# Performance work log

Hardware: AMD Instinct MI355X
Metric: run time of the kernel (lower is better)

Reference implementation:

```python
import jax, jax.numpy as jnp
import numpy as np
from jax import lax

D_MODEL = 512
NUM_HEADS = 8
HEADDIM = D_MODEL // NUM_HEADS      # 64
EXPAND = 2
D_INNER = EXPAND * D_MODEL          # 1024
D_STATE = 64
NGROUPS = 1
KCONV = 4                           # window_size -> depthwise conv kernel
NHEADS = D_INNER // HEADDIM         # 16 SSM heads
D_FF = 2048
CONV_DIM = D_INNER + 2 * NGROUPS * D_STATE          # 1152 (x, B, C)
D_IN_PROJ = 2 * D_INNER + 2 * NGROUPS * D_STATE + NHEADS  # 2192 (z, x, B, C, dt)
EPS = 1e-6


def _rmsnorm(x, eps=EPS):
    return x * lax.rsqrt(jnp.mean(x * x, axis=-1, keepdims=True) + eps)


def _silu(x):
    return x * jax.nn.sigmoid(x)


def _ssm_scan(xs, dt, A, Bm, Cm):
    # xs: [B,L,H,P], dt: [B,L,H], A: [H], Bm/Cm: [B,L,N]  (ngroups=1 broadcast over heads)
    dA = jnp.exp(dt * A)                 # [B,L,H] decay per step
    dBx = dt[..., None] * xs             # [B,L,H,P] input contribution
    h0 = jnp.zeros((xs.shape[0], xs.shape[2], xs.shape[3], Bm.shape[2]), xs.dtype)

    def step(h, t):
        dA_t, dBx_t, B_t, C_t = t        # [B,H],[B,H,P],[B,N],[B,N]
        h = dA_t[..., None, None] * h + dBx_t[..., None] * B_t[:, None, None, :]
        y = jnp.einsum('bhpn,bn->bhp', h, C_t)
        return h, y

    _, ys = lax.scan(step, h0, (dA.transpose(1, 0, 2), dBx.transpose(1, 0, 2, 3),
                                Bm.transpose(1, 0, 2), Cm.transpose(1, 0, 2)))
    return ys.transpose(1, 0, 2, 3)      # [B,L,H,P]


def setup_inputs() -> dict:
    key = jax.random.key(0)
    ks = jax.random.split(key, 12)
    B, L = 8, 2048
    s = 0.02
    inp = {
        'x': jax.random.normal(ks[0], (B, L, D_MODEL), jnp.float32),
        'mask': jnp.ones((B, L), jnp.float32),
        'W_in': jax.random.normal(ks[1], (D_MODEL, D_IN_PROJ), jnp.float32) * s,
        'conv_w': jax.random.normal(ks[2], (CONV_DIM, KCONV), jnp.float32) * 0.1,
        'conv_b': jnp.zeros((CONV_DIM,), jnp.float32),
        'dt_bias': jax.random.normal(ks[3], (NHEADS,), jnp.float32) * 0.1,
        'A_log': jnp.log(jnp.arange(1, NHEADS + 1, dtype=jnp.float32)),
        'D': jnp.ones((NHEADS,), jnp.float32),
        'norm_w': jnp.ones((D_INNER,), jnp.float32),
        'W_out': jax.random.normal(ks[4], (D_INNER, D_MODEL), jnp.float32) * s,
        'W1': jax.random.normal(ks[5], (D_MODEL, D_FF), jnp.float32) * s,
        'b1': jnp.zeros((D_FF,), jnp.float32),
        'W2': jax.random.normal(ks[6], (D_FF, D_MODEL), jnp.float32) * s,
        'b2': jnp.zeros((D_MODEL,), jnp.float32),
    }
    return inp


def reference(x, mask, W_in, conv_w, conv_b, dt_bias, A_log, D, norm_w, W_out, W1, b1, W2, b2):
    B, L, _ = x.shape
    x = x * mask[..., None]
    u = _rmsnorm(x)

    zxbcdt = u @ W_in                                   # [B,L,2192]
    z = zxbcdt[..., :D_INNER]
    xBC = zxbcdt[..., D_INNER:D_INNER + CONV_DIM]
    dt = zxbcdt[..., D_INNER + CONV_DIM:]               # [B,L,H]

    # causal depthwise conv1d, kernel KCONV
    pad = jnp.pad(xBC, ((0, 0), (KCONV - 1, 0), (0, 0)))
    xBC = sum(pad[:, i:i + L, :] * conv_w[:, i] for i in range(KCONV)) + conv_b
    xBC = _silu(xBC) * mask[..., None]

    xs = xBC[..., :D_INNER].reshape(B, L, NHEADS, HEADDIM)
    Bm = xBC[..., D_INNER:D_INNER + D_STATE]            # [B,L,N] (ngroups=1)
    Cm = xBC[..., D_INNER + D_STATE:]

    dt = jax.nn.softplus(dt + dt_bias)
    A = -jnp.exp(A_log)                                 # [H]

    # bidirectional (non-causal) selective scan: forward + reversed scans
    y_f = _ssm_scan(xs, dt, A, Bm, Cm)
    y_b = _ssm_scan(xs[:, ::-1], dt[:, ::-1], A, Bm[:, ::-1], Cm[:, ::-1])[:, ::-1]
    y = y_f + y_b + D[None, None, :, None] * xs         # [B,L,H,P]
    y = y.reshape(B, L, D_INNER)

    # gated RMSNorm then output projection
    y = _rmsnorm(y * _silu(z)) * norm_w
    m = y @ W_out                                       # mamba2 output, [B,L,D]

    x = m + m                                           # x = x + dropout1(x) with x := mamba out
    h = _rmsnorm(x)
    x = x + (jax.nn.gelu(h @ W1 + b1) @ W2 + b2)        # x + mlp(norm2(x))
    return (x, m, dt, z)
```

## Files before the change

kernel.cpp:

```cpp
#include <hip/hip_runtime.h>
#include <cstdint>
#include <cstddef>

#define L_SEQ   2048
#define NROWS   16384
#define D_MODEL 512
#define D_INNER 1024
#define D_STATE 64
#define NHEADS  16
#define CONV_DIM 1152
#define D_IN_PROJ 2192
#define D_FF 2048
#define EPS 1e-6f

typedef __bf16 bf16_t;
typedef __bf16 bf16x8 __attribute__((ext_vector_type(8)));
typedef float  f32x4  __attribute__((ext_vector_type(4)));

#define OFF_WT_IN    0ull
#define OFF_WT_OUT   2244608ull
#define OFF_W1T      3293184ull
#define OFF_W2T      5390336ull
#define OFF_U        7487488ull
#define OFF_XBC_RAW  24264704ull
#define OFF_XBC_CONV 99762176ull
#define OFF_Y2       175259648ull
#define OFF_YN       242368512ull

__device__ __forceinline__ void gl_lds16(const void* g, void* s) {
  __builtin_amdgcn_global_load_lds(
      (__attribute__((address_space(1))) void*)(void*)g,
      (__attribute__((address_space(3))) void*)s, 16, 0, 0);
}

__device__ __forceinline__ float block_sum256(float v, float* red) {
#pragma unroll
  for (int o = 32; o > 0; o >>= 1) v += __shfl_xor(v, o, 64);
  int w = threadIdx.x >> 6;
  if ((threadIdx.x & 63) == 0) red[w] = v;
  __syncthreads();
  return red[0] + red[1] + red[2] + red[3];
}

__device__ __forceinline__ float softplus_f(float x) {
  return (x > 20.f) ? x : log1pf(expf(x));
}
__device__ __forceinline__ float silu_f(float x) {
  return x / (1.f + expf(-x));
}
__device__ __forceinline__ float gelu_tanh_f(float x) {
  float x3 = x * x * x;
  return 0.5f * x * (1.f + tanhf(0.7978845608f * (x + 0.044715f * x3)));
}

__global__ __launch_bounds__(256) void prep_weights_kernel(
    const float* __restrict__ W_in, const float* __restrict__ W_out,
    const float* __restrict__ W1, const float* __restrict__ W2,
    bf16_t* __restrict__ wt_in, bf16_t* __restrict__ wt_out,
    bf16_t* __restrict__ w1t, bf16_t* __restrict__ w2t) {
  const int S1 = D_IN_PROJ * 512;
  const int S2 = 512 * 1024;
  const int S3 = 2048 * 512;
  const int S4 = 512 * 2048;
  const int total = S1 + S2 + S3 + S4;
  for (int i = blockIdx.x * 256 + threadIdx.x; i < total; i += gridDim.x * 256) {
    if (i < S1) {
      int n = i / 512, k = i - n * 512;
      wt_in[i] = (bf16_t)W_in[k * D_IN_PROJ + n];
    } else if (i < S1 + S2) {
      int j = i - S1; int n = j >> 10, k = j & 1023;
      wt_out[j] = (bf16_t)W_out[k * 512 + n];
    } else if (i < S1 + S2 + S3) {
      int j = i - S1 - S2; int n = j >> 9, k = j & 511;
      w1t[j] = (bf16_t)W1[k * 2048 + n];
    } else {
      int j = i - S1 - S2 - S3; int n = j >> 11, k = j & 2047;
      w2t[j] = (bf16_t)W2[k * 512 + n];
    }
  }
}

__global__ __launch_bounds__(256) void rmsnorm_in_kernel(
    const float* __restrict__ x, const float* __restrict__ mask,
    bf16_t* __restrict__ u) {
  __shared__ float red[4];
  int row = blockIdx.x;
  float mk = mask[row];
  const float* xr = x + (size_t)row * 512;
  float v0 = xr[threadIdx.x] * mk;
  float v1 = xr[threadIdx.x + 256] * mk;
  float ss = block_sum256(v0 * v0 + v1 * v1, red);
  float r = rsqrtf(ss * (1.f / 512.f) + EPS);
  bf16_t* ur = u + (size_t)row * 512;
  ur[threadIdx.x] = (bf16_t)(v0 * r);
  ur[threadIdx.x + 256] = (bf16_t)(v1 * r);
}

__global__ __launch_bounds__(256) void rmsnorm2_kernel(
    const float* __restrict__ m, bf16_t* __restrict__ h) {
  __shared__ float red[4];
  int row = blockIdx.x;
  const float* mr = m + (size_t)row * 512;
  float v0 = 2.f * mr[threadIdx.x];
  float v1 = 2.f * mr[threadIdx.x + 256];
  float ss = block_sum256(v0 * v0 + v1 * v1, red);
  float r = rsqrtf(ss * (1.f / 512.f) + EPS);
  bf16_t* hr = h + (size_t)row * 512;
  hr[threadIdx.x] = (bf16_t)(v0 * r);
  hr[threadIdx.x + 256] = (bf16_t)(v1 * r);
}

template <int EPI>
__global__ __launch_bounds__(256, 2) void gemm_kernel(
    const bf16_t* __restrict__ A, const bf16_t* __restrict__ Bt,
    int M, int N, int K,
    float* __restrict__ o0, float* __restrict__ o1, float* __restrict__ o2,
    bf16_t* __restrict__ ob, const float* __restrict__ bias,
    const float* __restrict__ extra) {
  __shared__ bf16_t As[128 * 32];
  __shared__ bf16_t Bs[128 * 32];
  const int tid = threadIdx.x;
  const int lane = tid & 63;
  const int w = tid >> 6;
  const int tileM = blockIdx.y * 128;
  const int tileN = blockIdx.x * 128;

  f32x4 acc[4][4] = {};

  const int wm = (w >> 1) * 64;
  const int wn = (w & 1) * 64;
  const int fr = lane & 15;
  const int fk = (lane >> 4) * 8;

  for (int k0 = 0; k0 < K; k0 += 32) {
    __syncthreads();
#pragma unroll
    for (int i = 0; i < 2; ++i) {
      int rloc = w * 32 + i * 16 + (lane >> 2);
      int cb = (lane & 3) * 16;
      const char* ga = (const char*)(A + (size_t)(tileM + rloc) * K + k0) + cb;
      gl_lds16(ga, (void*)&As[(w * 32 + i * 16) * 32]);
      int rn = tileN + rloc;
      if (rn >= N) rn = N - 1;
      const char* gb = (const char*)(Bt + (size_t)rn * K + k0) + cb;
      gl_lds16(gb, (void*)&Bs[(w * 32 + i * 16) * 32]);
    }
    __syncthreads();

    bf16x8 av[4], bv[4];
#pragma unroll
    for (int i = 0; i < 4; ++i)
      av[i] = *(const bf16x8*)&As[(wm + i * 16 + fr) * 32 + fk];
#pragma unroll
    for (int j = 0; j < 4; ++j)
      bv[j] = *(const bf16x8*)&Bs[(wn + j * 16 + fr) * 32 + fk];
#pragma unroll
    for (int i = 0; i < 4; ++i)
#pragma unroll
      for (int j = 0; j < 4; ++j)
        acc[i][j] = __builtin_amdgcn_mfma_f32_16x16x32_bf16(av[i], bv[j], acc[i][j], 0, 0, 0);
  }

  const int cn = lane & 15;
  const int r0 = (lane >> 4) * 4;
#pragma unroll
  for (int i = 0; i < 4; ++i) {
#pragma unroll
    for (int j = 0; j < 4; ++j) {
      int gn = tileN + wn + j * 16 + cn;
      if (gn >= N) continue;
#pragma unroll
      for (int r = 0; r < 4; ++r) {
        int gm = tileM + wm + i * 16 + r0 + r;
        float v = acc[i][j][r];
        if (EPI == 0) {
          o0[(size_t)gm * N + gn] = v;
        } else if (EPI == 1) {
          if (gn < D_INNER) {
            o0[(size_t)gm * D_INNER + gn] = v;
          } else if (gn < D_INNER + CONV_DIM) {
            o1[(size_t)gm * CONV_DIM + (gn - D_INNER)] = v;
          } else {
            int hh = gn - (D_INNER + CONV_DIM);
            o2[(size_t)gm * NHEADS + hh] = softplus_f(v + bias[hh]);
          }
        } else if (EPI == 2) {
          ob[(size_t)gm * N + gn] = (bf16_t)gelu_tanh_f(v + bias[gn]);
        } else if (EPI == 3) {
          o0[(size_t)gm * N + gn] = v + bias[gn] + 2.f * extra[(size_t)gm * N + gn];
        }
      }
    }
  }
}

__global__ __launch_bounds__(384) void conv_silu_kernel(
    const float* __restrict__ xbc_raw, const float* __restrict__ conv_w,
    const float* __restrict__ conv_b, const float* __restrict__ mask,
    float* __restrict__ xbc_conv) {
  int row = blockIdx.x;
  int t = row & (L_SEQ - 1);
  float mk = mask[row];
#pragma unroll
  for (int k = 0; k < 3; ++k) {
    int c = threadIdx.x + k * 384;
    float4 wv = ((const float4*)conv_w)[c];
    float acc = conv_b[c];
    if (t >= 3) acc += wv.x * xbc_raw[(size_t)(row - 3) * CONV_DIM + c];
    if (t >= 2) acc += wv.y * xbc_raw[(size_t)(row - 2) * CONV_DIM + c];
    if (t >= 1) acc += wv.z * xbc_raw[(size_t)(row - 1) * CONV_DIM + c];
    acc += wv.w * xbc_raw[(size_t)row * CONV_DIM + c];
    xbc_conv[(size_t)row * CONV_DIM + c] = silu_f(acc) * mk;
  }
}


__global__ __launch_bounds__(256) void scan_chunk_kernel(
    const float* __restrict__ xbc, const float* __restrict__ dt_all,
    const float* __restrict__ A_log,
    bf16_t* __restrict__ y2, bf16_t* __restrict__ Tc_buf,
    float* __restrict__ la_buf) {
  const int bid = blockIdx.x;
  const int c = bid & 31, h = (bid >> 5) & 15, b = (bid >> 9) & 7, dir = bid >> 12;
  const float A_h = -expf(A_log[h]);
  const int tid = threadIdx.x, w = tid >> 6, lane = tid & 63;
  const int fr = lane & 15, fk = (lane >> 4) * 8;

  __shared__ __align__(16) bf16_t sB[64][72];
  __shared__ __align__(16) bf16_t sC[64][72];
  __shared__ __align__(16) bf16_t sXt[64][72];
  __shared__ __align__(16) bf16_t sBwt[64][72];
  __shared__ float sLa[64], sDt[64], sW[64];

  const size_t base = (size_t)b * L_SEQ;
#define ROWOF(i) (base + (size_t)(dir ? (L_SEQ - 1 - (c * 64 + (i))) : (c * 64 + (i))))

  if (tid < 64) sDt[tid] = dt_all[ROWOF(tid) * NHEADS + h];

  float bB[16];
#pragma unroll
  for (int r = 0; r < 16; ++r) {
    int i = w * 16 + r;
    const float* src = xbc + ROWOF(i) * CONV_DIM;
    float xv = src[h * 64 + lane];
    float bv = src[D_INNER + lane];
    float cv = src[D_INNER + D_STATE + lane];
    bB[r] = bv;
    sB[i][lane] = (bf16_t)bv;
    sC[i][lane] = (bf16_t)cv;
    sXt[lane][i] = (bf16_t)xv;
  }
  __syncthreads();

  if (w == 0) {
    float v = sDt[lane] * A_h;
#pragma unroll
    for (int d = 1; d < 64; d <<= 1) {
      float o = __shfl_up(v, d, 64);
      if (lane >= d) v += o;
    }
    sLa[lane] = v;
    float la63 = __shfl(v, 63, 64);
    sW[lane] = __expf(la63 - v) * sDt[lane];
  }
  __syncthreads();

#pragma unroll
  for (int r = 0; r < 16; ++r) {
    int i = w * 16 + r;
    sBwt[lane][i] = (bf16_t)(bB[r] * sW[i]);
  }
  if (tid < 64) la_buf[(size_t)bid * 64 + tid] = sLa[tid];

  f32x4 acc1[4] = {};
#pragma unroll
  for (int k0 = 0; k0 < 64; k0 += 32) {
    bf16x8 bv = *(const bf16x8*)&sC[w * 16 + fr][k0 + fk];
#pragma unroll
    for (int mi = 0; mi < 4; ++mi) {
      if (mi <= w) {
        bf16x8 av = *(const bf16x8*)&sB[mi * 16 + fr][k0 + fk];
        acc1[mi] = __builtin_amdgcn_mfma_f32_16x16x32_bf16(av, bv, acc1[mi], 0, 0, 0);
      }
    }
  }
  __syncthreads();

  {
    bf16_t (*sM)[72] = sB;
    float la_t = sLa[w * 16 + fr];
    int t = w * 16 + fr;
#pragma unroll
    for (int mi = 0; mi < 4; ++mi) {
#pragma unroll
      for (int r = 0; r < 4; ++r) {
        int s = mi * 16 + (lane >> 4) * 4 + r;
        float mv = 0.f;
        if (s <= t) mv = acc1[mi][r] * __expf(la_t - sLa[s]) * sDt[s];
        sM[t][s] = (bf16_t)mv;
      }
    }
  }

  f32x4 acc3[4] = {};
#pragma unroll
  for (int k0 = 0; k0 < 64; k0 += 32) {
    bf16x8 bv = *(const bf16x8*)&sBwt[w * 16 + fr][k0 + fk];
#pragma unroll
    for (int mi = 0; mi < 4; ++mi) {
      bf16x8 av = *(const bf16x8*)&sXt[mi * 16 + fr][k0 + fk];
      acc3[mi] = __builtin_amdgcn_mfma_f32_16x16x32_bf16(av, bv, acc3[mi], 0, 0, 0);
    }
  }
  __syncthreads();

  f32x4 acc2[4] = {};
  {
    bf16_t (*sM)[72] = sB;
#pragma unroll
    for (int k0 = 0; k0 < 64; k0 += 32) {
      bf16x8 bv = *(const bf16x8*)&sXt[w * 16 + fr][k0 + fk];
#pragma unroll
      for (int mi = 0; mi < 4; ++mi) {
        bf16x8 av = *(const bf16x8*)&sM[mi * 16 + fr][k0 + fk];
        acc2[mi] = __builtin_amdgcn_mfma_f32_16x16x32_bf16(av, bv, acc2[mi], 0, 0, 0);
      }
    }
  }

  bf16_t* yout = y2 + (size_t)dir * NROWS * D_INNER;
  bf16_t* tco = Tc_buf + (size_t)bid * 4096;
#pragma unroll
  for (int mi = 0; mi < 4; ++mi) {
#pragma unroll
    for (int r = 0; r < 4; ++r) {
      int rowl = mi * 16 + (lane >> 4) * 4 + r;
      int coll = w * 16 + fr;
      yout[ROWOF(rowl) * D_INNER + h * 64 + coll] = (bf16_t)acc2[mi][r];
      tco[rowl * 64 + coll] = (bf16_t)acc3[mi][r];
    }
  }
#undef ROWOF
}

__global__ __launch_bounds__(256) void state_prefix_kernel(
    const float* __restrict__ la_buf, bf16_t* __restrict__ Tc_buf) {
  const int g = blockIdx.x >> 1;
  const int e0 = (blockIdx.x & 1) * 2048 + threadIdx.x * 8;
  bf16_t* tc = Tc_buf + (size_t)g * 32 * 4096 + e0;
  const float* la63 = la_buf + (size_t)g * 32 * 64 + 63;
  float S[8] = {};
  for (int cc = 0; cc < 32; ++cc) {
    bf16x8 t = *(const bf16x8*)(tc + (size_t)cc * 4096);
    float d = __expf(la63[cc * 64]);
    bf16_t sb[8];
#pragma unroll
    for (int j = 0; j < 8; ++j) sb[j] = (bf16_t)S[j];
    *(bf16x8*)(tc + (size_t)cc * 4096) = *(bf16x8*)sb;
    const bf16_t* tp = (const bf16_t*)&t;
#pragma unroll
    for (int j = 0; j < 8; ++j) S[j] = d * S[j] + (float)tp[j];
  }
}

__global__ __launch_bounds__(256) void ystate_kernel(
    const float* __restrict__ xbc, const bf16_t* __restrict__ S_buf,
    const float* __restrict__ la_buf, bf16_t* __restrict__ y2) {
  const int bid = blockIdx.x;
  const int c = bid & 31, h = (bid >> 5) & 15, b = (bid >> 9) & 7, dir = bid >> 12;
  const int tid = threadIdx.x, w = tid >> 6, lane = tid & 63;
  const int fr = lane & 15, fk = (lane >> 4) * 8;
  const size_t base = (size_t)b * L_SEQ;

  const bf16_t* Sp = S_buf + (size_t)bid * 4096;
  f32x4 acc[4] = {};
#pragma unroll
  for (int k0 = 0; k0 < 64; k0 += 32) {
    bf16x8 bv = *(const bf16x8*)&Sp[(w * 16 + fr) * 64 + k0 + fk];
#pragma unroll
    for (int mi = 0; mi < 4; ++mi) {
      int t = c * 64 + mi * 16 + fr;
      int tr = dir ? (L_SEQ - 1 - t) : t;
      const float* cp = xbc + (base + tr) * CONV_DIM + D_INNER + D_STATE + k0 + fk;
      bf16_t av[8];
#pragma unroll
      for (int j = 0; j < 8; ++j) av[j] = (bf16_t)cp[j];
      acc[mi] = __builtin_amdgcn_mfma_f32_16x16x32_bf16(*(bf16x8*)av, bv, acc[mi], 0, 0, 0);
    }
  }
  const float* la = la_buf + (size_t)bid * 64;
  bf16_t* yout = y2 + (size_t)dir * NROWS * D_INNER;
  const int p = w * 16 + fr;
#pragma unroll
  for (int mi = 0; mi < 4; ++mi) {
#pragma unroll
    for (int r = 0; r < 4; ++r) {
      int tl = mi * 16 + (lane >> 4) * 4 + r;
      int t = c * 64 + tl;
      int tr = dir ? (L_SEQ - 1 - t) : t;
      size_t g = (base + tr) * D_INNER + h * 64 + p;
      float v = acc[mi][r] * __expf(la[tl]);
      yout[g] = (bf16_t)((float)yout[g] + v);
    }
  }
}

__global__ __launch_bounds__(256) void combine_kernel(
    const bf16_t* __restrict__ y2, const float* __restrict__ xbc_conv,
    const float* __restrict__ z, const float* __restrict__ Dp,
    const float* __restrict__ norm_w, bf16_t* __restrict__ yn) {
  __shared__ float red[4];
  int row = blockIdx.x;
  const bf16_t* yf = y2 + (size_t)row * D_INNER;
  const bf16_t* yb = y2 + (size_t)NROWS * D_INNER + (size_t)row * D_INNER;
  const float* xs = xbc_conv + (size_t)row * CONV_DIM;
  const float* zr = z + (size_t)row * D_INNER;

  float g[4];
  float ss = 0.f;
#pragma unroll
  for (int k = 0; k < 4; ++k) {
    int c = threadIdx.x + k * 256;
    float v = (float)yf[c] + (float)yb[c] + Dp[c >> 6] * xs[c];
    float gg = v * silu_f(zr[c]);
    g[k] = gg;
    ss += gg * gg;
  }
  ss = block_sum256(ss, red);
  float r = rsqrtf(ss * (1.f / 1024.f) + EPS);
  bf16_t* yr = yn + (size_t)row * D_INNER;
#pragma unroll
  for (int k = 0; k < 4; ++k) {
    int c = threadIdx.x + k * 256;
    yr[c] = (bf16_t)(g[k] * r * norm_w[c]);
  }
}

extern "C" void kernel_launch(void* const* d_in, const int* in_sizes, int n_in,
                              void* d_out, int out_size, void* d_ws, size_t ws_size,
                              hipStream_t stream) {
  const float* x       = (const float*)d_in[0];
  const float* mask    = (const float*)d_in[1];
  const float* W_in    = (const float*)d_in[2];
  const float* conv_w  = (const float*)d_in[3];
  const float* conv_b  = (const float*)d_in[4];
  const float* dt_bias = (const float*)d_in[5];
  const float* A_log   = (const float*)d_in[6];
  const float* Dp      = (const float*)d_in[7];
  const float* norm_w  = (const float*)d_in[8];
  const float* W_out   = (const float*)d_in[9];
  const float* W1      = (const float*)d_in[10];
  const float* b1      = (const float*)d_in[11];
  const float* W2      = (const float*)d_in[12];
  const float* b2      = (const float*)d_in[13];

  float* out_x  = (float*)d_out;
  float* out_m  = out_x + (size_t)NROWS * 512;
  float* out_dt = out_m + (size_t)NROWS * 512;
  float* out_z  = out_dt + (size_t)NROWS * NHEADS;

  char* ws = (char*)d_ws;
  bf16_t* wt_in    = (bf16_t*)(ws + OFF_WT_IN);
  bf16_t* wt_out   = (bf16_t*)(ws + OFF_WT_OUT);
  bf16_t* w1t      = (bf16_t*)(ws + OFF_W1T);
  bf16_t* w2t      = (bf16_t*)(ws + OFF_W2T);
  bf16_t* u_bf     = (bf16_t*)(ws + OFF_U);
  float*  xbc_raw  = (float*)(ws + OFF_XBC_RAW);
  float*  xbc_conv = (float*)(ws + OFF_XBC_CONV);
  bf16_t* y2       = (bf16_t*)(ws + OFF_Y2);
  bf16_t* yn       = (bf16_t*)(ws + OFF_YN);
  bf16_t* h_bf     = u_bf;
  bf16_t* gelu_bf  = (bf16_t*)(ws + OFF_XBC_RAW);
  bf16_t* Tc_buf   = (bf16_t*)(ws + OFF_XBC_RAW);
  float*  la_buf   = (float*)(ws + OFF_U);

  prep_weights_kernel<<<14624, 256, 0, stream>>>(W_in, W_out, W1, W2, wt_in, wt_out, w1t, w2t);
  rmsnorm_in_kernel<<<NROWS, 256, 0, stream>>>(x, mask, u_bf);
  gemm_kernel<1><<<dim3(18, 128), 256, 0, stream>>>(u_bf, wt_in, NROWS, D_IN_PROJ, 512,
                                                    out_z, xbc_raw, out_dt, nullptr, dt_bias, nullptr);
  conv_silu_kernel<<<NROWS, 384, 0, stream>>>(xbc_raw, conv_w, conv_b, mask, xbc_conv);
  scan_chunk_kernel<<<8192, 256, 0, stream>>>(xbc_conv, out_dt, A_log, y2, Tc_buf, la_buf);
  state_prefix_kernel<<<512, 256, 0, stream>>>(la_buf, Tc_buf);
  ystate_kernel<<<8192, 256, 0, stream>>>(xbc_conv, Tc_buf, la_buf, y2);
  combine_kernel<<<NROWS, 256, 0, stream>>>(y2, xbc_conv, out_z, Dp, norm_w, yn);
  gemm_kernel<0><<<dim3(4, 128), 256, 0, stream>>>(yn, wt_out, NROWS, 512, 1024,
                                                   out_m, nullptr, nullptr, nullptr, nullptr, nullptr);
  rmsnorm2_kernel<<<NROWS, 256, 0, stream>>>(out_m, h_bf);
  gemm_kernel<2><<<dim3(16, 128), 256, 0, stream>>>(h_bf, w1t, NROWS, D_FF, 512,
                                                    nullptr, nullptr, nullptr, gelu_bf, b1, nullptr);
  gemm_kernel<3><<<dim3(4, 128), 256, 0, stream>>>(gelu_bf, w2t, NROWS, 512, D_FF,
                                                   out_x, nullptr, nullptr, nullptr, b2, out_m);
}
```

Baseline: 728.9 us.

## Stage C tile in LDS, reuse across four heads, and vectorize y updates

The ystate kernel now loads the C tile for each chunk into shared memory once, converts it to bf16, and reuses it for four heads per block. Previously each block reread and converted C from global memory for a single head. Results are staged through an LDS buffer so the read-modify-write of y2 uses coalesced 16-byte accesses instead of scattered scalar bf16 accesses. The grid shrinks by a factor of four, which lowers parallelism and adds extra barriers per head.

```diff
diff --git a/kernel.cpp b/kernel.cpp
--- a/kernel.cpp
+++ b/kernel.cpp
@@ -15,6 +15,7 @@
 
 typedef __bf16 bf16_t;
 typedef __bf16 bf16x8 __attribute__((ext_vector_type(8)));
+typedef __bf16 bf16x4 __attribute__((ext_vector_type(4)));
 typedef float  f32x4  __attribute__((ext_vector_type(4)));
 
 #define OFF_WT_IN    0ull
@@ -367,40 +368,72 @@
     const float* __restrict__ xbc, const bf16_t* __restrict__ S_buf,
     const float* __restrict__ la_buf, bf16_t* __restrict__ y2) {
   const int bid = blockIdx.x;
-  const int c = bid & 31, h = (bid >> 5) & 15, b = (bid >> 9) & 7, dir = bid >> 12;
+  const int hg = bid & 3, c = (bid >> 2) & 31, b = (bid >> 7) & 7, dir = bid >> 10;
   const int tid = threadIdx.x, w = tid >> 6, lane = tid & 63;
   const int fr = lane & 15, fk = (lane >> 4) * 8;
   const size_t base = (size_t)b * L_SEQ;
 
-  const bf16_t* Sp = S_buf + (size_t)bid * 4096;
-  f32x4 acc[4] = {};
-#pragma unroll
-  for (int k0 = 0; k0 < 64; k0 += 32) {
-    bf16x8 bv = *(const bf16x8*)&Sp[(w * 16 + fr) * 64 + k0 + fk];
+  __shared__ __align__(16) bf16_t sC[64][72];
+  __shared__ __align__(16) float  sYf[64][72];
+  __shared__ float sEla[64];
+
+#pragma unroll
+  for (int uu = 0; uu < 4; ++uu) {
+    int u = tid + uu * 256;
+    int row = u >> 4, q = u & 15;
+    int t = c * 64 + row;
+    int tr = dir ? (L_SEQ - 1 - t) : t;
+    float4 cv = *(const float4*)(xbc + (base + tr) * CONV_DIM + D_INNER + D_STATE + q * 4);
+    bf16x4 cb;
+    cb[0] = (bf16_t)cv.x; cb[1] = (bf16_t)cv.y; cb[2] = (bf16_t)cv.z; cb[3] = (bf16_t)cv.w;
+    *(bf16x4*)&sC[row][q * 4] = cb;
+  }
+  __syncthreads();
+
+  bf16_t* yout = y2 + (size_t)dir * NROWS * D_INNER;
+
+#pragma unroll 1
+  for (int hi = 0; hi < 4; ++hi) {
+    const int h = hg * 4 + hi;
+    const int bidh = dir * 4096 + b * 512 + h * 32 + c;
+    if (tid < 64) sEla[tid] = __expf(la_buf[(size_t)bidh * 64 + tid]);
+
+    const bf16_t* Sp = S_buf + (size_t)bidh * 4096;
+    f32x4 acc[4] = {};
+#pragma unroll
+    for (int k0 = 0; k0 < 64; k0 += 32) {
+      bf16x8 bv = *(const bf16x8*)(Sp + (w * 16 + fr) * 64 + k0 + fk);
+#pragma unroll
+      for (int mi = 0; mi < 4; ++mi) {
+        bf16x8 av = *(const bf16x8*)&sC[mi * 16 + fr][k0 + fk];
+        acc[mi] = __builtin_amdgcn_mfma_f32_16x16x32_bf16(av, bv, acc[mi], 0, 0, 0);
+      }
+    }
+    __syncthreads();
+
 #pragma unroll
     for (int mi = 0; mi < 4; ++mi) {
-      int t = c * 64 + mi * 16 + fr;
+#pragma unroll
+      for (int r = 0; r < 4; ++r) {
+        int tl = mi * 16 + (lane >> 4) * 4 + r;
+        sYf[tl][w * 16 + fr] = acc[mi][r] * sEla[tl];
+      }
+    }
+    __syncthreads();
+
+#pragma unroll
+    for (int uu = 0; uu < 2; ++uu) {
+      int u = tid + uu * 256;
+      int row = u >> 3, oct = u & 7;
+      int t = c * 64 + row;
       int tr = dir ? (L_SEQ - 1 - t) : t;
-      const float* cp = xbc + (base + tr) * CONV_DIM + D_INNER + D_STATE + k0 + fk;
-      bf16_t av[8];
-#pragma unroll
-      for (int j = 0; j < 8; ++j) av[j] = (bf16_t)cp[j];
-      acc[mi] = __builtin_amdgcn_mfma_f32_16x16x32_bf16(*(bf16x8*)av, bv, acc[mi], 0, 0, 0);
-    }
-  }
-  const float* la = la_buf + (size_t)bid * 64;
-  bf16_t* yout = y2 + (size_t)dir * NROWS * D_INNER;
-  const int p = w * 16 + fr;
-#pragma unroll
-  for (int mi = 0; mi < 4; ++mi) {
-#pragma unroll
-    for (int r = 0; r < 4; ++r) {
-      int tl = mi * 16 + (lane >> 4) * 4 + r;
-      int t = c * 64 + tl;
-      int tr = dir ? (L_SEQ - 1 - t) : t;
-      size_t g = (base + tr) * D_INNER + h * 64 + p;
-      float v = acc[mi][r] * __expf(la[tl]);
-      yout[g] = (bf16_t)((float)yout[g] + v);
+      bf16_t* gp = yout + (base + tr) * D_INNER + h * 64 + oct * 8;
+      bf16x8 old = *(const bf16x8*)gp;
+      const float* yp = &sYf[row][oct * 8];
+      bf16x8 nw;
+#pragma unroll
+      for (int j = 0; j < 8; ++j) nw[j] = (bf16_t)((float)old[j] + yp[j]);
+      *(bf16x8*)gp = nw;
     }
   }
 }
@@ -481,7 +514,7 @@
   conv_silu_kernel<<<NROWS, 384, 0, stream>>>(xbc_raw, conv_w, conv_b, mask, xbc_conv);
   scan_chunk_kernel<<<8192, 256, 0, stream>>>(xbc_conv, out_dt, A_log, y2, Tc_buf, la_buf);
   state_prefix_kernel<<<512, 256, 0, stream>>>(la_buf, Tc_buf);
-  ystate_kernel<<<8192, 256, 0, stream>>>(xbc_conv, Tc_buf, la_buf, y2);
+  ystate_kernel<<<2048, 256, 0, stream>>>(xbc_conv, Tc_buf, la_buf, y2);
   combine_kernel<<<NROWS, 256, 0, stream>>>(y2, xbc_conv, out_z, Dp, norm_w, yn);
   gemm_kernel<0><<<dim3(4, 128), 256, 0, stream>>>(yn, wt_out, NROWS, 512, 1024,
                                                    out_m, nullptr, nullptr, nullptr, nullptr, nullptr);
```

After: 677.3 us. 7.1% less time.
